# Performance work log

Measured on AMD Instinct MI355X. Metric: run time of the kernel, lower is better.

## Reference

```python
import jax, jax.numpy as jnp
import numpy as np
from jax import lax

B, S, D, H, HFF, T = 256, 33, 42, 128, 256, 20
BN_EPS = 1e-5

def _bn(x, g, b):
    # eval-mode BatchNorm1d with running_mean=0, running_var=1
    return x * (g / jnp.sqrt(1.0 + BN_EPS)) + b

def _gelu(x):
    return jax.nn.gelu(x, approximate=False)  # torch default GELU (exact)

def setup_inputs() -> dict:
    key = jax.random.key(0)
    ks = iter(jax.random.split(key, 48))
    w = lambda shp, s=0.02: jax.random.normal(next(ks), shp, dtype=jnp.float32) * s
    z = lambda shp: jnp.zeros(shp, jnp.float32)
    o = lambda shp: jnp.ones(shp, jnp.float32)
    inp = {
        'interaction_path': jax.random.normal(next(ks), (B, S, D), dtype=jnp.float32),
        'timestamps': jnp.broadcast_to(jnp.arange(S, dtype=jnp.float32) * 0.1, (B, S)),
        # initial encoder: Linear(42->128), BN, GELU, Linear(128->128), BN
        'enc_w1': w((D, H)), 'enc_b1': z(H), 'enc_g1': o(H), 'enc_be1': z(H),
        'enc_w2': w((H, H)), 'enc_b2': z(H), 'enc_g2': o(H), 'enc_be2': z(H),
        # vector field: 128->256 (BN,GELU), 256->256 (BN,GELU) x2, 256->5376
        'vf_w0': w((H, HFF)), 'vf_b0': z(HFF), 'vf_g0': o(HFF), 'vf_be0': z(HFF),
        'vf_w1': w((HFF, HFF)), 'vf_b1': z(HFF), 'vf_g1': o(HFF), 'vf_be1': z(HFF),
        'vf_w2': w((HFF, HFF)), 'vf_b2': z(HFF), 'vf_g2': o(HFF), 'vf_be2': z(HFF),
        'vf_w3': w((HFF, H * D)), 'vf_b3': z(H * D),
        # multihead attention (seq_len = 1 -> softmax is identically 1)
        'wv': w((H, H)), 'bv': z(H), 'wo': w((H, H)), 'bo': z(H),
        # 20 trait decoders, stacked: 128->64->32->1
        'dw1': w((T, H, 64)), 'db1': z((T, 64)),
        'dw2': w((T, 64, 32)), 'db2': z((T, 32)),
        'dw3': w((T, 32, 1)), 'db3': z((T, 1)),
    }
    return inp

def reference(interaction_path, timestamps,
              enc_w1, enc_b1, enc_g1, enc_be1, enc_w2, enc_b2, enc_g2, enc_be2,
              vf_w0, vf_b0, vf_g0, vf_be0, vf_w1, vf_b1, vf_g1, vf_be1,
              vf_w2, vf_b2, vf_g2, vf_be2, vf_w3, vf_b3,
              wv, bv, wo, bo,
              dw1, db1, dw2, db2, dw3, db3):
    b = interaction_path.shape[0]
    # ---- initial encoder on X[:, 0] ----
    x0 = interaction_path[:, 0]                      # [B, D]
    h = _gelu(_bn(x0 @ enc_w1 + enc_b1, enc_g1, enc_be1))
    z0 = _bn(h @ enc_w2 + enc_b2, enc_g2, enc_be2)   # [B, H]

    # ---- CDE vector field: z -> [B, H, D] ----
    def vf(zz):
        y = _gelu(_bn(zz @ vf_w0 + vf_b0, vf_g0, vf_be0))
        y = _gelu(_bn(y @ vf_w1 + vf_b1, vf_g1, vf_be1))
        y = _gelu(_bn(y @ vf_w2 + vf_b2, vf_g2, vf_be2))
        return (y @ vf_w3 + vf_b3).reshape(b, H, D)

    def g(zz, dxdt):  # f(z) @ dX/dt  -> [B, H]
        return jnp.einsum('bhd,bd->bh', vf(zz), dxdt)

    # linear-interpolation control path: piecewise-constant derivative
    t = timestamps[0]                                # [S]
    dt = t[1:] - t[:-1]                              # [S-1]
    dX = interaction_path[:, 1:] - interaction_path[:, :-1]   # [B, S-1, D]
    dXdt = dX / dt[None, :, None]                    # [B, S-1, D]

    def step(zz, x):
        dxdt, hstep = x
        k1 = g(zz, dxdt)
        k2 = g(zz + 0.5 * hstep * k1, dxdt)
        k3 = g(zz + 0.5 * hstep * k2, dxdt)
        k4 = g(zz + hstep * k3, dxdt)
        return zz + (hstep / 6.0) * (k1 + 2.0 * k2 + 2.0 * k3 + k4), None

    zT, _ = lax.scan(step, z0, (jnp.swapaxes(dXdt, 0, 1), dt))  # [B, H]

    # ---- self-attention over a length-1 sequence: softmax==1 -> out_proj(v) ----
    attended = (zT @ wv + bv) @ wo + bo              # [B, H]

    # ---- 20 trait decoders (stacked / vectorized) ----
    h1 = _gelu(jnp.einsum('bh,thd->tbd', attended, dw1) + db1[:, None, :])
    h2 = _gelu(jnp.einsum('tbd,tde->tbe', h1, dw2) + db2[:, None, :])
    out = jax.nn.sigmoid(jnp.einsum('tbe,teo->tbo', h2, dw3) + db3[:, None, :])
    return jnp.transpose(out[..., 0], (1, 0))        # [B, 20]
```

## Files before the change

kernel.cpp:

```cpp
#include <hip/hip_runtime.h>
#include <cstdint>

constexpr int B    = 256;
constexpr int S    = 33;
constexpr int D    = 42;
constexpr int H    = 128;
constexpr int HFF  = 256;
constexpr int T    = 20;
constexpr int NSTEP = S - 1;
constexpr int DP   = D / 2;
constexpr int ADW  = 8192;
constexpr int CH   = 16;
constexpr int NCH  = NSTEP / CH;
#define BN_SCALE 0.9999950000374997f

typedef _Float16 h2v __attribute__((ext_vector_type(2)));
typedef _Float16 f16x8 __attribute__((ext_vector_type(8)));
typedef float    f32x4 __attribute__((ext_vector_type(4)));
union UH2 { uint32_t u; h2v h; };

__device__ __forceinline__ float fdot2u(uint32_t a, uint32_t b, float c) {
    UH2 x, y; x.u = a; y.u = b;
    return __builtin_amdgcn_fdot2(x.h, y.h, c, false);
}
__device__ __forceinline__ uint32_t packh2(float a, float b) {
    UH2 u; u.h = h2v{(_Float16)a, (_Float16)b}; return u.u;
}
__device__ __forceinline__ float gelu_exact(float x) {
    return 0.5f * x * (1.0f + erff(x * 0.70710678118654752f));
}
__device__ __forceinline__ float gelu_fast(float x) {
    float inner = x * (1.0f + 0.044715f * x * x);
    float E = __expf(1.5957691216f * inner);
    return x * E * __frcp_rn(E + 1.0f);
}
__device__ __forceinline__ int aswz(int idx) {
    return (idx & ~31) | ((idx & 31) ^ (((idx >> 9) & 3) << 1));
}

__global__ void pack_kernel(const float* __restrict__ w0, const float* __restrict__ w1,
                            const float* __restrict__ w2, const float* __restrict__ w3,
                            uint32_t* __restrict__ wcol, uint32_t* __restrict__ wp) {
    int idx = blockIdx.x * 256 + threadIdx.x;
    if (idx < 160 * 512) {
        int r = idx >> 9, t = idx & 511;
        int j = t >> 1, half = t & 1;
        float a, bb;
        if (r < 32)      { int ip = half * 32 + r;      a = w0[(2*ip)*HFF + j]; bb = w0[(2*ip+1)*HFF + j]; }
        else if (r < 96) { int ip = half * 64 + (r-32); a = w1[(2*ip)*HFF + j]; bb = w1[(2*ip+1)*HFF + j]; }
        else             { int ip = half * 64 + (r-96); a = w2[(2*ip)*HFF + j]; bb = w2[(2*ip+1)*HFF + j]; }
        wcol[idx] = packh2(a, bb);
    }
    if (idx < 32768 * 32) {
        int m = idx >> 5, dd = (idx & 31) * 2;
        int e = 4 * (m >> 9) + (m & 3);
        int h = (m >> 2) & 127;
        const float* row = w3 + (size_t)e * (H * D) + h * D;
        float a = (dd     < D) ? row[dd]     : 0.f;
        float b = (dd + 1 < D) ? row[dd + 1] : 0.f;
        wp[idx] = packh2(a, b);
    }
}

__global__ void prep_kernel(const float* __restrict__ path, const float* __restrict__ ts,
                            const float* __restrict__ ew1, const float* __restrict__ eb1,
                            const float* __restrict__ eg1, const float* __restrict__ ebe1,
                            const float* __restrict__ ew2, const float* __restrict__ eb2,
                            const float* __restrict__ eg2, const float* __restrict__ ebe2,
                            const float* __restrict__ b3,
                            float* __restrict__ zbuf, uint32_t* __restrict__ dxp,
                            float* __restrict__ bd3g, float* __restrict__ dtb) {
    __shared__ float x0[D], hb[H], dxs[NSTEP][D];
    int b = blockIdx.x, tid = threadIdx.x;
    if (tid < D) x0[tid] = path[b * S * D + tid];
    __syncthreads();
    {
        float acc = eb1[tid];
        for (int d = 0; d < D; ++d) acc += x0[d] * ew1[d * H + tid];
        hb[tid] = gelu_exact(acc * (eg1[tid] * BN_SCALE) + ebe1[tid]);
    }
    __syncthreads();
    {
        float acc = eb2[tid];
        for (int i = 0; i < H; ++i) acc += hb[i] * ew2[i * H + tid];
        zbuf[b * H + tid] = acc * (eg2[tid] * BN_SCALE) + ebe2[tid];
    }
    for (int idx = tid; idx < NSTEP * 32; idx += 128) {
        int s = idx >> 5, j2 = idx & 31;
        uint32_t val = 0;
        if (j2 < DP) {
            float dtv = ts[s + 1] - ts[s];
            int base = b * S * D + s * D + 2 * j2;
            float v0 = (path[base + D] - path[base]) / dtv;
            float v1 = (path[base + D + 1] - path[base + 1]) / dtv;
            dxs[s][2 * j2] = v0; dxs[s][2 * j2 + 1] = v1;
            val = packh2(v0, v1);
        }
        dxp[((size_t)(s * B + b)) * 32 + j2] = val;
    }
    __syncthreads();
    for (int s = 0; s < NSTEP; ++s) {
        float a = 0.f;
        for (int d = 0; d < D; ++d) a += b3[tid * D + d] * dxs[s][d];
        bd3g[(size_t)(s * B + b) * H + tid] = a;
    }
    if (b == 0 && tid < NSTEP) dtb[tid] = ts[tid + 1] - ts[tid];
}

__global__ void __launch_bounds__(256) amm_kernel(
    const uint32_t* __restrict__ wp, const uint32_t* __restrict__ dxp,
    uint32_t* __restrict__ Ach, int s0) {
    __shared__ __align__(16) uint32_t xpose[4][16 * 36];
    int t = threadIdx.x;
    int l = t & 63, wid = t >> 6;
    int mg = (blockIdx.x & 63) * 4 + wid;
    int sg = blockIdx.x >> 6;
    int lr = l & 15, lk = l >> 4;
    const char* wpB = (const char*)wp;
    const char* dxB = (const char*)dxp + (size_t)s0 * B * 128;
    char* asB = (char*)Ach;
    uint32_t* xp = xpose[wid];
    f16x8 af0[8], af1[8];
#pragma unroll
    for (int mi = 0; mi < 8; ++mi) {
        const f16x8* p = (const f16x8*)(wpB + ((size_t)(mg * 8 + mi) * 16 + lr) * 128 + lk * 16);
        af0[mi] = p[0]; af1[mi] = p[4];
    }
#pragma unroll
    for (int si = 0; si < 8; ++si) {
        int q = sg * 128 + si * 16 + lr;
#pragma unroll
        for (int mi = 0; mi < 8; ++mi) {
            const f16x8* bp = (const f16x8*)(dxB + (size_t)q * 128 + lk * 16);
            f16x8 b0 = bp[0], b1 = bp[4];
            f32x4 acc = {0.f, 0.f, 0.f, 0.f};
            acc = __builtin_amdgcn_mfma_f32_16x16x32_f16(af0[mi], b0, acc, 0, 0, 0);
            acc = __builtin_amdgcn_mfma_f32_16x16x32_f16(af1[mi], b1, acc, 0, 0, 0);
            uint32_t P0 = packh2(acc[0], acc[1]) + 0x00800080u;
            uint32_t P1 = packh2(acc[2], acc[3]) + 0x00800080u;
            uint32_t Q = __builtin_amdgcn_perm(P1, P0, 0x07050301u);
            xp[lr * 36 + lk + 4 * mi] = Q;
        }
        __syncthreads();
        {
            int qr = l >> 2, seg = l & 3;
            const uint4* src = (const uint4*)(xp + qr * 36 + seg * 8);
            uint4 v0 = src[0], v1 = src[1];
            int qout = sg * 128 + si * 16 + qr;
            char* outB = asB + (size_t)qout * 32768 + mg * 128 + seg * 32;
            *(uint4*)outB = v0;
            *(uint4*)(outB + 16) = v1;
        }
        __syncthreads();
    }
}

__global__ void __launch_bounds__(512, 1)
__attribute__((amdgpu_waves_per_eu(2, 8)))
scan_kernel(
    const uint32_t* __restrict__ wcol, const uint32_t* __restrict__ Ach,
    const float* __restrict__ vb0, const float* __restrict__ vg0, const float* __restrict__ vbe0,
    const float* __restrict__ vb1, const float* __restrict__ vg1, const float* __restrict__ vbe1,
    const float* __restrict__ vb2, const float* __restrict__ vg2, const float* __restrict__ vbe2,
    const float* __restrict__ bd3g, const float* __restrict__ dtb,
    float* __restrict__ zbuf, int s0) {
    __shared__ __align__(16) uint32_t ABUF[2][ADW];
    __shared__ __align__(16) uint32_t zzPd[72];
    __shared__ __align__(16) uint32_t yA[136], yB[136], yC[136];
    int t = threadIdx.x, b = blockIdx.x;
    int j = t >> 1, half = t & 1;
    int h = t >> 2, g = t & 3;
    int hswz = h ^ (g << 3);
    uint32_t w0h[32], w1h[64], w2h[64];
#pragma unroll
    for (int r = 0; r < 32; ++r) w0h[r] = wcol[r * 512 + t];
#pragma unroll
    for (int r = 0; r < 64; ++r) w1h[r] = wcol[(32 + r) * 512 + t];
#pragma unroll
    for (int r = 0; r < 64; ++r) w2h[r] = wcol[(96 + r) * 512 + t];
    float c0s = vg0[j] * BN_SCALE, c0o = vb0[j] * c0s + vbe0[j];
    float c1s = vg1[j] * BN_SCALE, c1o = vb1[j] * c1s + vbe1[j];
    float c2s = vg2[j] * BN_SCALE, c2o = vb2[j] * c2s + vbe2[j];
    float zf = zbuf[b * H + h];
    {
        const uint4* Ag = (const uint4*)(Ach + (size_t)b * ADW);
        uint4 a0 = Ag[t], a1 = Ag[512 + t], a2 = Ag[1024 + t], a3 = Ag[1536 + t];
        uint4* Ad = (uint4*)ABUF[0];
        Ad[aswz(t)] = a0; Ad[aswz(512 + t)] = a1;
        Ad[aswz(1024 + t)] = a2; Ad[aswz(1536 + t)] = a3;
    }
    {
        float zhi = __shfl_down(zf, 4, 64);
        if ((t & 7) == 0) {
            int ip = t >> 3;
            zzPd[(ip >> 5) * 36 + (ip & 31)] = packh2(zf, zhi);
        }
    }
    __syncthreads();

    for (int sl = 0; sl < CH; ++sl) {
        int s = s0 + sl;
        float hstep = dtb[s];
        float bd3 = bd3g[(size_t)(s * B + b) * H + h];
        uint4 pf0, pf1, pf2, pf3;
        {
            int sn = (sl + 1 < CH) ? sl + 1 : sl;
            const uint4* Ag = (const uint4*)(Ach + (size_t)(sn * B + b) * ADW);
            pf0 = Ag[t]; pf1 = Ag[512 + t]; pf2 = Ag[1024 + t]; pf3 = Ag[1536 + t];
        }
        const uint32_t* AL = ABUF[sl & 1];
        float ksum = 0.f, kcur = 0.f;
        for (int r = 0; r < 4; ++r) {
            {
                float pa = 0.f, pb = 0.f, pc = 0.f, pd = 0.f;
                const uint4* zq = (const uint4*)(zzPd + half * 36);
#pragma unroll
                for (int u4 = 0; u4 < 8; ++u4) {
                    uint4 zv = zq[u4];
                    pa = fdot2u(w0h[4*u4+0], zv.x, pa); pb = fdot2u(w0h[4*u4+1], zv.y, pb);
                    pc = fdot2u(w0h[4*u4+2], zv.z, pc); pd = fdot2u(w0h[4*u4+3], zv.w, pd);
                }
                float p = (pa + pb) + (pc + pd);
                p += __shfl_xor(p, 1, 64);
                float v = gelu_fast(p * c0s + c0o);
                float vhi = __shfl_down(v, 2, 64);
                if ((t & 3) == 0) {
                    int ip = t >> 2;
                    yA[(ip >> 6) * 68 + (ip & 63)] = packh2(v, vhi);
                }
            }
            __syncthreads();
            {
                float pa = 0.f, pb = 0.f, pc = 0.f, pd = 0.f;
                const uint4* yq = (const uint4*)(yA + half * 68);
#pragma unroll
                for (int u4 = 0; u4 < 16; ++u4) {
                    uint4 yv = yq[u4];
                    pa = fdot2u(w1h[4*u4+0], yv.x, pa); pb = fdot2u(w1h[4*u4+1], yv.y, pb);
                    pc = fdot2u(w1h[4*u4+2], yv.z, pc); pd = fdot2u(w1h[4*u4+3], yv.w, pd);
                }
                float p = (pa + pb) + (pc + pd);
                p += __shfl_xor(p, 1, 64);
                float v = gelu_fast(p * c1s + c1o);
                float vhi = __shfl_down(v, 2, 64);
                if ((t & 3) == 0) {
                    int ip = t >> 2;
                    yB[(ip >> 6) * 68 + (ip & 63)] = packh2(v, vhi);
                }
            }
            __syncthreads();
            {
                float pa = 0.f, pb = 0.f, pc = 0.f, pd = 0.f;
                const uint4* yq = (const uint4*)(yB + half * 68);
#pragma unroll
                for (int u4 = 0; u4 < 16; ++u4) {
                    uint4 yv = yq[u4];
                    pa = fdot2u(w2h[4*u4+0], yv.x, pa); pb = fdot2u(w2h[4*u4+1], yv.y, pb);
                    pc = fdot2u(w2h[4*u4+2], yv.z, pc); pd = fdot2u(w2h[4*u4+3], yv.w, pd);
                }
                float p = (pa + pb) + (pc + pd);
                p += __shfl_xor(p, 1, 64);
                float v = gelu_fast(p * c2s + c2o);
                float vhi = __shfl_down(v, 2, 64);
                if ((t & 3) == 0) {
                    int ip = t >> 2;
                    yC[(ip >> 6) * 68 + (ip & 63)] = packh2(v, vhi);
                }
            }
            __syncthreads();
            {
                float pA = 0.f, pB = 0.f, pC = 0.f, pD = 0.f;
                int ybase = (g >> 1) * 68 + (g & 1) * 32;
                const uint4* yq = (const uint4*)(yC + ybase);
#pragma unroll
                for (int kk = 0; kk < 8; ++kk) {
                    uint4 yv = yq[kk];
                    int k0 = g * 16 + 2 * kk;
                    uint32_t Qa = AL[k0 * 128 + hswz];
                    uint32_t Qb = AL[(k0 + 1) * 128 + hswz];
                    pA = fdot2u(__builtin_amdgcn_perm(0u, Qa, 0x010C000Cu), yv.x, pA);
                    pB = fdot2u(__builtin_amdgcn_perm(0u, Qa, 0x030C020Cu), yv.y, pB);
                    pC = fdot2u(__builtin_amdgcn_perm(0u, Qb, 0x010C000Cu), yv.z, pC);
                    pD = fdot2u(__builtin_amdgcn_perm(0u, Qb, 0x030C020Cu), yv.w, pD);
                }
                float ptot = (pA + pB) + (pC + pD);
                ptot += __shfl_xor(ptot, 1, 64);
                ptot += __shfl_xor(ptot, 2, 64);
                kcur = bd3 + ptot;
                float wsm = (r == 1 || r == 2) ? 2.f : 1.f;
                ksum += wsm * kcur;
                float zz;
                if (r < 3) {
                    float cin = (r == 2) ? 1.f : 0.5f;
                    zz = zf + cin * hstep * kcur;
                } else {
                    zf += hstep * (1.f / 6.f) * ksum;
                    zz = zf;
                }
                float zhi = __shfl_down(zz, 4, 64);
                if ((t & 7) == 0) {
                    int ip = t >> 3;
                    zzPd[(ip >> 5) * 36 + (ip & 31)] = packh2(zz, zhi);
                }
            }
            if (r == 3) {
                uint4* Ad = (uint4*)ABUF[(sl + 1) & 1];
                Ad[aswz(t)] = pf0; Ad[aswz(512 + t)] = pf1;
                Ad[aswz(1024 + t)] = pf2; Ad[aswz(1536 + t)] = pf3;
            }
            __syncthreads();
        }
    }
    if ((t & 3) == 0) zbuf[b * H + h] = zf;
}

__global__ void att_kernel(const float* __restrict__ zbuf,
                           const float* __restrict__ wv, const float* __restrict__ bv,
                           const float* __restrict__ wo, const float* __restrict__ bo,
                           float* __restrict__ att) {
    __shared__ float zl[H], v[H];
    int b = blockIdx.x, tid = threadIdx.x;
    zl[tid] = zbuf[b * H + tid];
    __syncthreads();
    {
        float acc = bv[tid];
#pragma unroll 8
        for (int i = 0; i < H; ++i) acc += zl[i] * wv[i * H + tid];
        v[tid] = acc;
    }
    __syncthreads();
    {
        float acc = bo[tid];
#pragma unroll 8
        for (int i = 0; i < H; ++i) acc += v[i] * wo[i * H + tid];
        att[b * H + tid] = acc;
    }
}

__global__ void __launch_bounds__(64) dec_kernel(
    const float* __restrict__ att,
    const float* __restrict__ dw1, const float* __restrict__ db1,
    const float* __restrict__ dw2, const float* __restrict__ db2,
    const float* __restrict__ dw3, const float* __restrict__ db3,
    float* __restrict__ out) {
    int bid = blockIdx.x;
    int t = bid >> 8, b = bid & 255;
    int tid = threadIdx.x;
    __shared__ float al[H], h1l[64];
    al[tid] = att[b * H + tid];
    al[tid + 64] = att[b * H + tid + 64];
    __syncthreads();
    {
        float acc = db1[t * 64 + tid];
#pragma unroll 8
        for (int i = 0; i < H; ++i) acc += al[i] * dw1[t * H * 64 + i * 64 + tid];
        h1l[tid] = gelu_exact(acc);
    }
    __syncthreads();
    float v = 0.f;
    if (tid < 32) {
        float acc = db2[t * 32 + tid];
#pragma unroll 8
        for (int i = 0; i < 64; ++i) acc += h1l[i] * dw2[t * 64 * 32 + i * 32 + tid];
        v = gelu_exact(acc) * dw3[t * 32 + tid];
    }
#pragma unroll
    for (int off = 16; off >= 1; off >>= 1) v += __shfl_down(v, off, 64);
    if (tid == 0) out[b * T + t] = 1.f / (1.f + expf(-(v + db3[t])));
}

extern "C" void kernel_launch(void* const* d_in, const int* in_sizes, int n_in,
                              void* d_out, int out_size, void* d_ws, size_t ws_size,
                              hipStream_t stream) {
    const float* path = (const float*)d_in[0];
    const float* ts   = (const float*)d_in[1];
    const float* ew1  = (const float*)d_in[2];
    const float* eb1  = (const float*)d_in[3];
    const float* eg1  = (const float*)d_in[4];
    const float* ebe1 = (const float*)d_in[5];
    const float* ew2  = (const float*)d_in[6];
    const float* eb2  = (const float*)d_in[7];
    const float* eg2  = (const float*)d_in[8];
    const float* ebe2 = (const float*)d_in[9];
    const float* vw0  = (const float*)d_in[10];
    const float* vb0  = (const float*)d_in[11];
    const float* vg0  = (const float*)d_in[12];
    const float* vbe0 = (const float*)d_in[13];
    const float* vw1  = (const float*)d_in[14];
    const float* vb1  = (const float*)d_in[15];
    const float* vg1  = (const float*)d_in[16];
    const float* vbe1 = (const float*)d_in[17];
    const float* vw2  = (const float*)d_in[18];
    const float* vb2  = (const float*)d_in[19];
    const float* vg2  = (const float*)d_in[20];
    const float* vbe2 = (const float*)d_in[21];
    const float* vw3  = (const float*)d_in[22];
    const float* vb3  = (const float*)d_in[23];
    const float* wv   = (const float*)d_in[24];
    const float* bv   = (const float*)d_in[25];
    const float* wo   = (const float*)d_in[26];
    const float* bo   = (const float*)d_in[27];
    const float* dw1  = (const float*)d_in[28];
    const float* db1  = (const float*)d_in[29];
    const float* dw2  = (const float*)d_in[30];
    const float* db2  = (const float*)d_in[31];
    const float* dw3  = (const float*)d_in[32];
    const float* db3  = (const float*)d_in[33];

    char* ws = (char*)d_ws;
    size_t off = 0;
    auto take = [&](size_t bytes) { char* p = ws + off; off += (bytes + 255) & ~(size_t)255; return p; };
    uint32_t* Ach   = (uint32_t*)take((size_t)CH * B * ADW * 4);
    uint32_t* dxp   = (uint32_t*)take((size_t)NSTEP * B * 32 * 4);
    float*    bd3g  = (float*)take((size_t)NSTEP * B * H * 4);
    float*    dtb   = (float*)take(NSTEP * 4);
    float*    zbuf  = (float*)take((size_t)B * H * 4);
    float*    att   = (float*)take((size_t)B * H * 4);
    uint32_t* wcol  = (uint32_t*)take((size_t)160 * 512 * 4);
    uint32_t* wp    = (uint32_t*)take((size_t)32768 * 32 * 4);

    pack_kernel<<<(32768 * 32 + 255) / 256, 256, 0, stream>>>(vw0, vw1, vw2, vw3, wcol, wp);
    prep_kernel<<<B, 128, 0, stream>>>(path, ts, ew1, eb1, eg1, ebe1,
                                       ew2, eb2, eg2, ebe2, vb3, zbuf, dxp, bd3g, dtb);
    for (int c = 0; c < NCH; ++c) {
        amm_kernel<<<2048, 256, 0, stream>>>(wp, dxp, Ach, c * CH);
        scan_kernel<<<B, 512, 0, stream>>>(wcol, Ach,
                                           vb0, vg0, vbe0, vb1, vg1, vbe1, vb2, vg2, vbe2,
                                           bd3g, dtb, zbuf, c * CH);
    }
    att_kernel<<<B, 128, 0, stream>>>(zbuf, wv, bv, wo, bo, att);
    dec_kernel<<<T * B, 64, 0, stream>>>(att, dw1, db1, dw2, db2, dw3, db3, (float*)d_out);
}
```

Baseline: 550.6 us.

## Split MLP dot products four ways per output pair in scan kernel

Each thread now computes two adjacent output neurons over a quarter of the input dimension, instead of one neuron over half of it. The packed weight layout and the shared-memory activation layouts are reorganized to match. Each thread reads half as many LDS vectors per layer, and outputs are written as paired uint2 stores by fewer threads. The cost is one extra cross-lane shuffle level per reduction, and the new index mappings must stay consistent with the pack kernel.

Result: slower. 589.7 us (+7.1%).

```diff
diff --git a/kernel.cpp b/kernel.cpp
--- a/kernel.cpp
+++ b/kernel.cpp
@@ -44,11 +44,21 @@
     int idx = blockIdx.x * 256 + threadIdx.x;
     if (idx < 160 * 512) {
         int r = idx >> 9, t = idx & 511;
-        int j = t >> 1, half = t & 1;
+        int jp = t >> 2, q4 = t & 3;
         float a, bb;
-        if (r < 32)      { int ip = half * 32 + r;      a = w0[(2*ip)*HFF + j]; bb = w0[(2*ip+1)*HFF + j]; }
-        else if (r < 96) { int ip = half * 64 + (r-32); a = w1[(2*ip)*HFF + j]; bb = w1[(2*ip+1)*HFF + j]; }
-        else             { int ip = half * 64 + (r-96); a = w2[(2*ip)*HFF + j]; bb = w2[(2*ip+1)*HFF + j]; }
+        if (r < 32) {
+            int os = r >> 4, ipq = r & 15;
+            int ip = q4 * 16 + ipq, o = 2 * jp + os;
+            a = w0[(2*ip)*HFF + o]; bb = w0[(2*ip+1)*HFF + o];
+        } else if (r < 96) {
+            int rr = r - 32, os = rr >> 5, ipq = rr & 31;
+            int ip = q4 * 32 + ipq, o = 2 * jp + os;
+            a = w1[(2*ip)*HFF + o]; bb = w1[(2*ip+1)*HFF + o];
+        } else {
+            int rr = r - 96, os = rr >> 5, ipq = rr & 31;
+            int ip = q4 * 32 + ipq, o = 2 * jp + os;
+            a = w2[(2*ip)*HFF + o]; bb = w2[(2*ip+1)*HFF + o];
+        }
         wcol[idx] = packh2(a, bb);
     }
     if (idx < 32768 * 32) {
@@ -165,10 +175,10 @@
     const float* __restrict__ bd3g, const float* __restrict__ dtb,
     float* __restrict__ zbuf, int s0) {
     __shared__ __align__(16) uint32_t ABUF[2][ADW];
-    __shared__ __align__(16) uint32_t zzPd[72];
-    __shared__ __align__(16) uint32_t yA[136], yB[136], yC[136];
+    __shared__ __align__(16) uint32_t zzPd[80];
+    __shared__ __align__(16) uint32_t yA[144], yB[144], yC[144];
     int t = threadIdx.x, b = blockIdx.x;
-    int j = t >> 1, half = t & 1;
+    int jp = t >> 2, q4 = t & 3;
     int h = t >> 2, g = t & 3;
     int hswz = h ^ (g << 3);
     uint32_t w0h[32], w1h[64], w2h[64];
@@ -178,9 +188,13 @@
     for (int r = 0; r < 64; ++r) w1h[r] = wcol[(32 + r) * 512 + t];
 #pragma unroll
     for (int r = 0; r < 64; ++r) w2h[r] = wcol[(96 + r) * 512 + t];
-    float c0s = vg0[j] * BN_SCALE, c0o = vb0[j] * c0s + vbe0[j];
-    float c1s = vg1[j] * BN_SCALE, c1o = vb1[j] * c1s + vbe1[j];
-    float c2s = vg2[j] * BN_SCALE, c2o = vb2[j] * c2s + vbe2[j];
+    int o0 = 2 * jp, o1 = 2 * jp + 1;
+    float c0s0 = vg0[o0] * BN_SCALE, c0o0 = vb0[o0] * c0s0 + vbe0[o0];
+    float c0s1 = vg0[o1] * BN_SCALE, c0o1 = vb0[o1] * c0s1 + vbe0[o1];
+    float c1s0 = vg1[o0] * BN_SCALE, c1o0 = vb1[o0] * c1s0 + vbe1[o0];
+    float c1s1 = vg1[o1] * BN_SCALE, c1o1 = vb1[o1] * c1s1 + vbe1[o1];
+    float c2s0 = vg2[o0] * BN_SCALE, c2o0 = vb2[o0] * c2s0 + vbe2[o0];
+    float c2s1 = vg2[o1] * BN_SCALE, c2o1 = vb2[o1] * c2s1 + vbe2[o1];
     float zf = zbuf[b * H + h];
     {
         const uint4* Ag = (const uint4*)(Ach + (size_t)b * ADW);
@@ -191,9 +205,12 @@
     }
     {
         float zhi = __shfl_down(zf, 4, 64);
-        if ((t & 7) == 0) {
-            int ip = t >> 3;
-            zzPd[(ip >> 5) * 36 + (ip & 31)] = packh2(zf, zhi);
+        uint32_t pk = packh2(zf, zhi);
+        uint32_t pk2 = (uint32_t)__shfl_down((int)pk, 8, 64);
+        if ((t & 15) == 0) {
+            int d = t >> 3;
+            uint2 u; u.x = pk; u.y = pk2;
+            *(uint2*)&zzPd[(d >> 4) * 20 + (d & 15)] = u;
         }
     }
     __syncthreads();
@@ -212,66 +229,80 @@
         float ksum = 0.f, kcur = 0.f;
         for (int r = 0; r < 4; ++r) {
             {
-                float pa = 0.f, pb = 0.f, pc = 0.f, pd = 0.f;
-                const uint4* zq = (const uint4*)(zzPd + half * 36);
-#pragma unroll
-                for (int u4 = 0; u4 < 8; ++u4) {
+                float p0a = 0.f, p0b = 0.f, p1a = 0.f, p1b = 0.f;
+                const uint4* zq = (const uint4*)(zzPd + q4 * 20);
+#pragma unroll
+                for (int u4 = 0; u4 < 4; ++u4) {
                     uint4 zv = zq[u4];
-                    pa = fdot2u(w0h[4*u4+0], zv.x, pa); pb = fdot2u(w0h[4*u4+1], zv.y, pb);
-                    pc = fdot2u(w0h[4*u4+2], zv.z, pc); pd = fdot2u(w0h[4*u4+3], zv.w, pd);
-                }
-                float p = (pa + pb) + (pc + pd);
-                p += __shfl_xor(p, 1, 64);
-                float v = gelu_fast(p * c0s + c0o);
-                float vhi = __shfl_down(v, 2, 64);
-                if ((t & 3) == 0) {
-                    int ip = t >> 2;
-                    yA[(ip >> 6) * 68 + (ip & 63)] = packh2(v, vhi);
+                    p0a = fdot2u(w0h[u4*4+0], zv.x, p0a); p0b = fdot2u(w0h[u4*4+1], zv.y, p0b);
+                    p0a = fdot2u(w0h[u4*4+2], zv.z, p0a); p0b = fdot2u(w0h[u4*4+3], zv.w, p0b);
+                    p1a = fdot2u(w0h[16+u4*4+0], zv.x, p1a); p1b = fdot2u(w0h[16+u4*4+1], zv.y, p1b);
+                    p1a = fdot2u(w0h[16+u4*4+2], zv.z, p1a); p1b = fdot2u(w0h[16+u4*4+3], zv.w, p1b);
+                }
+                float p0 = p0a + p0b, p1 = p1a + p1b;
+                p0 += __shfl_xor(p0, 1, 64); p0 += __shfl_xor(p0, 2, 64);
+                p1 += __shfl_xor(p1, 1, 64); p1 += __shfl_xor(p1, 2, 64);
+                float v0 = gelu_fast(p0 * c0s0 + c0o0);
+                float v1 = gelu_fast(p1 * c0s1 + c0o1);
+                uint32_t pk = packh2(v0, v1);
+                uint32_t pk2 = (uint32_t)__shfl_down((int)pk, 4, 64);
+                if ((t & 7) == 0) {
+                    uint2 u; u.x = pk; u.y = pk2;
+                    *(uint2*)&yA[(jp >> 5) * 36 + (jp & 31)] = u;
                 }
             }
             __syncthreads();
             {
-                float pa = 0.f, pb = 0.f, pc = 0.f, pd = 0.f;
-                const uint4* yq = (const uint4*)(yA + half * 68);
-#pragma unroll
-                for (int u4 = 0; u4 < 16; ++u4) {
+                float p0a = 0.f, p0b = 0.f, p1a = 0.f, p1b = 0.f;
+                const uint4* yq = (const uint4*)(yA + q4 * 36);
+#pragma unroll
+                for (int u4 = 0; u4 < 8; ++u4) {
                     uint4 yv = yq[u4];
-                    pa = fdot2u(w1h[4*u4+0], yv.x, pa); pb = fdot2u(w1h[4*u4+1], yv.y, pb);
-                    pc = fdot2u(w1h[4*u4+2], yv.z, pc); pd = fdot2u(w1h[4*u4+3], yv.w, pd);
-                }
-                float p = (pa + pb) + (pc + pd);
-                p += __shfl_xor(p, 1, 64);
-                float v = gelu_fast(p * c1s + c1o);
-                float vhi = __shfl_down(v, 2, 64);
-                if ((t & 3) == 0) {
-                    int ip = t >> 2;
-                    yB[(ip >> 6) * 68 + (ip & 63)] = packh2(v, vhi);
+                    p0a = fdot2u(w1h[u4*4+0], yv.x, p0a); p0b = fdot2u(w1h[u4*4+1], yv.y, p0b);
+                    p0a = fdot2u(w1h[u4*4+2], yv.z, p0a); p0b = fdot2u(w1h[u4*4+3], yv.w, p0b);
+                    p1a = fdot2u(w1h[32+u4*4+0], yv.x, p1a); p1b = fdot2u(w1h[32+u4*4+1], yv.y, p1b);
+                    p1a = fdot2u(w1h[32+u4*4+2], yv.z, p1a); p1b = fdot2u(w1h[32+u4*4+3], yv.w, p1b);
+                }
+                float p0 = p0a + p0b, p1 = p1a + p1b;
+                p0 += __shfl_xor(p0, 1, 64); p0 += __shfl_xor(p0, 2, 64);
+                p1 += __shfl_xor(p1, 1, 64); p1 += __shfl_xor(p1, 2, 64);
+                float v0 = gelu_fast(p0 * c1s0 + c1o0);
+                float v1 = gelu_fast(p1 * c1s1 + c1o1);
+                uint32_t pk = packh2(v0, v1);
+                uint32_t pk2 = (uint32_t)__shfl_down((int)pk, 4, 64);
+                if ((t & 7) == 0) {
+                    uint2 u; u.x = pk; u.y = pk2;
+                    *(uint2*)&yB[(jp >> 5) * 36 + (jp & 31)] = u;
                 }
             }
             __syncthreads();
             {
-                float pa = 0.f, pb = 0.f, pc = 0.f, pd = 0.f;
-                const uint4* yq = (const uint4*)(yB + half * 68);
-#pragma unroll
-                for (int u4 = 0; u4 < 16; ++u4) {
+                float p0a = 0.f, p0b = 0.f, p1a = 0.f, p1b = 0.f;
+                const uint4* yq = (const uint4*)(yB + q4 * 36);
+#pragma unroll
+                for (int u4 = 0; u4 < 8; ++u4) {
                     uint4 yv = yq[u4];
-                    pa = fdot2u(w2h[4*u4+0], yv.x, pa); pb = fdot2u(w2h[4*u4+1], yv.y, pb);
-                    pc = fdot2u(w2h[4*u4+2], yv.z, pc); pd = fdot2u(w2h[4*u4+3], yv.w, pd);
-                }
-                float p = (pa + pb) + (pc + pd);
-                p += __shfl_xor(p, 1, 64);
-                float v = gelu_fast(p * c2s + c2o);
-                float vhi = __shfl_down(v, 2, 64);
-                if ((t & 3) == 0) {
-                    int ip = t >> 2;
-                    yC[(ip >> 6) * 68 + (ip & 63)] = packh2(v, vhi);
+                    p0a = fdot2u(w2h[u4*4+0], yv.x, p0a); p0b = fdot2u(w2h[u4*4+1], yv.y, p0b);
+                    p0a = fdot2u(w2h[u4*4+2], yv.z, p0a); p0b = fdot2u(w2h[u4*4+3], yv.w, p0b);
+                    p1a = fdot2u(w2h[32+u4*4+0], yv.x, p1a); p1b = fdot2u(w2h[32+u4*4+1], yv.y, p1b);
+                    p1a = fdot2u(w2h[32+u4*4+2], yv.z, p1a); p1b = fdot2u(w2h[32+u4*4+3], yv.w, p1b);
+                }
+                float p0 = p0a + p0b, p1 = p1a + p1b;
+                p0 += __shfl_xor(p0, 1, 64); p0 += __shfl_xor(p0, 2, 64);
+                p1 += __shfl_xor(p1, 1, 64); p1 += __shfl_xor(p1, 2, 64);
+                float v0 = gelu_fast(p0 * c2s0 + c2o0);
+                float v1 = gelu_fast(p1 * c2s1 + c2o1);
+                uint32_t pk = packh2(v0, v1);
+                uint32_t pk2 = (uint32_t)__shfl_down((int)pk, 4, 64);
+                if ((t & 7) == 0) {
+                    uint2 u; u.x = pk; u.y = pk2;
+                    *(uint2*)&yC[(jp >> 5) * 36 + (jp & 31)] = u;
                 }
             }
             __syncthreads();
             {
                 float pA = 0.f, pB = 0.f, pC = 0.f, pD = 0.f;
-                int ybase = (g >> 1) * 68 + (g & 1) * 32;
-                const uint4* yq = (const uint4*)(yC + ybase);
+                const uint4* yq = (const uint4*)(yC + g * 36);
 #pragma unroll
                 for (int kk = 0; kk < 8; ++kk) {
                     uint4 yv = yq[kk];
@@ -298,9 +329,12 @@
                     zz = zf;
                 }
                 float zhi = __shfl_down(zz, 4, 64);
-                if ((t & 7) == 0) {
-                    int ip = t >> 3;
-                    zzPd[(ip >> 5) * 36 + (ip & 31)] = packh2(zz, zhi);
+                uint32_t pk = packh2(zz, zhi);
+                uint32_t pk2 = (uint32_t)__shfl_down((int)pk, 8, 64);
+                if ((t & 15) == 0) {
+                    int d = t >> 3;
+                    uint2 u; u.x = pk; u.y = pk2;
+                    *(uint2*)&zzPd[(d >> 4) * 20 + (d & 15)] = u;
                 }
             }
             if (r == 3) {
```
